# Optimization experiments

Measured on AMD Instinct MI355X. Metric: run time of the kernel, lower is better.

## Reference

```python
import jax, jax.numpy as jnp
import numpy as np

N_MEMORY = 16
FEA_DIM = 512


def setup_inputs() -> dict:
    key = jax.random.key(0)
    ks = jax.random.split(key, 8)
    b, L, d, n = 4, 4096, FEA_DIM, N_MEMORY
    scale = 1.0 / np.sqrt(d)  # ~ torch Linear default init scale
    return {
        "query": jax.random.normal(ks[0], (b, L, d), dtype=jnp.float32),
        "W1": jax.random.uniform(ks[1], (n, d, d), jnp.float32, -scale, scale),
        "b1": jax.random.uniform(ks[2], (n, d), jnp.float32, -scale, scale),
        "W2": jax.random.uniform(ks[3], (n, d, d), jnp.float32, -scale, scale),
        "b2": jax.random.uniform(ks[4], (n, d), jnp.float32, -scale, scale),
        "Wg": jax.random.uniform(ks[5], (n, d), jnp.float32, -scale, scale),
        "bg": jax.random.uniform(ks[6], (n,), jnp.float32, -scale, scale),
        "topk": 8,
    }


def reference(query, W1, b1, W2, b2, Wg, bg, topk):
    # query: [b, L, d]; stacked per-memory-slot params: W1/W2 [n, d, d], Wg [n, d]
    n = W1.shape[0]
    # per-slot LeakyReLU negative slopes: 0.01 + 0.2/n * l
    slopes = (0.01 + 0.2 / n * jnp.arange(n, dtype=query.dtype))[:, None, None, None]
    # memory_function: Linear -> LeakyReLU(slope_l) -> Linear -> Tanh, all slots at once
    h = jnp.einsum('bld,ndh->nblh', query, W1) + b1[:, None, None, :]   # [n,b,L,d]
    h = jnp.where(h >= 0, h, h * slopes)
    x = jnp.tanh(jnp.einsum('nblh,nhd->nbld', h, W2) + b2[:, None, None, :])  # [n,b,L,d]
    # gate: Linear(d,1) -> softmax over L -> topk over L -> gather -> weighted sum
    logits = jnp.einsum('nbld,nd->nbl', x, Wg) + bg[:, None, None]      # [n,b,L]
    w = jax.nn.softmax(logits, axis=-1)
    top_w, top_idx = jax.lax.top_k(w, topk)                             # [n,b,k]
    items = jnp.take_along_axis(x, top_idx[..., None], axis=2)          # [n,b,k,d]
    combined = jnp.einsum('nbkd,nbk->nbd', items, top_w)                # [n,b,d]
    m_item = jnp.transpose(combined, (1, 0, 2))                         # [b,n,d]
    # F.normalize(dim=-1), eps=1e-12
    norm = jnp.maximum(jnp.linalg.norm(m_item, axis=-1, keepdims=True), 1e-12)
    return m_item / norm
```

## Files before the change

kernel.cpp:

```cpp
#include <hip/hip_runtime.h>
#include <hip/hip_bf16.h>
#include <cstdint>
#include <cstddef>

#define NMEM 16
#define DDIM 512
#define BATCH 4
#define LSEQ 4096
#define ROWS 16384
#define NCAND 32
#define KTOP 8
#define QPAD 20

typedef __attribute__((ext_vector_type(4))) float f32x4;
typedef __attribute__((ext_vector_type(16))) float f32x16;
typedef __attribute__((ext_vector_type(8))) int int8v;

__device__ inline void gld16(const void* gptr, void* lptr) {
    __builtin_amdgcn_global_load_lds(
        (const __attribute__((address_space(1))) unsigned int*)gptr,
        (__attribute__((address_space(3))) unsigned int*)lptr,
        16, 0, 0);
}

__device__ inline float fast_tanh(float x) {
    float t = __builtin_amdgcn_fmed3f(x, -3.f, 3.f);
    float t2 = t * t;
    return t * (27.f + t2) * __builtin_amdgcn_rcpf(27.f + 9.f * t2);
}

__device__ inline int8v ldg_frag(const unsigned char* p) {
    int4 x = *(const int4*)p;
    int4 y = *(const int4*)(p + 16);
    int8v v;
    v[0] = x.x; v[1] = x.y; v[2] = x.z; v[3] = x.w;
    v[4] = y.x; v[5] = y.y; v[6] = y.z; v[7] = y.w;
    return v;
}

__device__ inline int8v load_frag_half(const unsigned char* Ts, int row, int kh) {
    int key = (row >> 1) & 3;
    const int4* p0 = (const int4*)(Ts + row * 64 + ((((kh << 1) | 0) ^ key) << 4));
    const int4* p1 = (const int4*)(Ts + row * 64 + ((((kh << 1) | 1) ^ key) << 4));
    int4 x = *p0, y = *p1;
    int8v v;
    v[0] = x.x; v[1] = x.y; v[2] = x.z; v[3] = x.w;
    v[4] = y.x; v[5] = y.y; v[6] = y.z; v[7] = y.w;
    return v;
}

__device__ inline void stage_half(const unsigned char* Wbase, unsigned char* dst,
                                  int tid) {
    #pragma unroll
    for (int i = 0; i < 2; ++i) {
        int c = i * 256 + tid;
        int row = c >> 2, s = c & 3;
        gld16(Wbase + (size_t)row * DDIM + ((s ^ ((row >> 1) & 3)) << 4),
              dst + c * 16);
    }
}

__global__ __launch_bounds__(256)
void prep_kernel(const float* __restrict__ query,
                 const float* __restrict__ W1, const float* __restrict__ W2,
                 unsigned char* __restrict__ Q8,
                 unsigned char* __restrict__ W1T8, unsigned char* __restrict__ W2T8) {
    int blk = blockIdx.x, t = threadIdx.x;
    if (blk < 2048) {
        size_t base = ((size_t)blk * 256 + t) * 16;
        const float4* in = (const float4*)(query + base);
        int4 o; int* op = (int*)&o;
        #pragma unroll
        for (int q = 0; q < 4; ++q) {
            float4 v = in[q];
            int lo = __builtin_amdgcn_cvt_pk_fp8_f32(v.x, v.y, 0, false);
            op[q] = __builtin_amdgcn_cvt_pk_fp8_f32(v.z, v.w, lo, true);
        }
        *(int4*)(Q8 + base) = o;
    } else {
        __shared__ float tile[64][69];
        int bid = blk - 2048;
        const float* Win = W1; unsigned char* Wout = W1T8;
        if (bid >= 1024) { bid -= 1024; Win = W2; Wout = W2T8; }
        int n = bid >> 6, t64 = bid & 63;
        int dt = (t64 >> 3) << 6, jt = (t64 & 7) << 6;
        const float* inN = Win + (size_t)n * DDIM * DDIM;
        unsigned char* outN = Wout + (size_t)n * DDIM * DDIM;
        int rr = t >> 4, cc = (t & 15) * 4;
        #pragma unroll
        for (int pass = 0; pass < 4; ++pass) {
            int row = rr + pass * 16;
            float4 v = *(const float4*)(inN + (size_t)(dt + row) * DDIM + jt + cc);
            tile[row][cc] = v.x; tile[row][cc + 1] = v.y;
            tile[row][cc + 2] = v.z; tile[row][cc + 3] = v.w;
        }
        __syncthreads();
        #pragma unroll
        for (int pass = 0; pass < 4; ++pass) {
            int jl = rr + pass * 16;
            float f0 = tile[cc][jl], f1 = tile[cc + 1][jl];
            float f2 = tile[cc + 2][jl], f3 = tile[cc + 3][jl];
            int lo = __builtin_amdgcn_cvt_pk_fp8_f32(f0, f1, 0, false);
            int dw = __builtin_amdgcn_cvt_pk_fp8_f32(f2, f3, lo, true);
            *(int*)(outN + (size_t)(jt + jl) * DDIM + dt + cc) = dw;
        }
    }
}

__global__ __launch_bounds__(256, 3)
void fused_mlp_kernel(const unsigned char* __restrict__ Q8,
                      const unsigned char* __restrict__ W1T8,
                      const unsigned char* __restrict__ W2T8,
                      const float* __restrict__ b1, const float* __restrict__ b2,
                      const float* __restrict__ Wg,
                      float* __restrict__ logits)
{
    __shared__ unsigned char hbuf[64 * 512];
    __shared__ unsigned char Bs[2][8192];
    __shared__ float lsum[2][64];
    const int id = blockIdx.x;
    const int n = id & 15;
    const int m0 = (id >> 4) * 64;
    const int tid = threadIdx.x, lane = tid & 63;
    const int w = tid >> 6;
    const int rh = w >> 1, ch = w & 1;
    const int l31 = lane & 31, kh = lane >> 5;
    const unsigned char* W1n = W1T8 + (size_t)n * DDIM * DDIM;
    const unsigned char* W2n = W2T8 + (size_t)n * DDIM * DDIM;
    const float slope = 0.01f + 0.0125f * n;
    const unsigned char* Aq0 = Q8 + (size_t)(m0 + rh * 32 + l31) * DDIM + kh * 32;

    int8v avq[8];
    #pragma unroll
    for (int qa = 0; qa < 8; ++qa)
        avq[qa] = ldg_frag(Aq0 + qa * 64);
    stage_half(W1n, Bs[0], tid);
    __syncthreads();

    #pragma unroll 1
    for (int n0 = 0; n0 < 4; ++n0) {
        f32x16 acc[2] = {};
        #pragma unroll
        for (int p8 = 0; p8 < 8; ++p8) {
            const int P = n0 * 8 + p8, Pn = P + 1;
            const unsigned char* nsrc = (Pn < 32)
                ? W1n + (size_t)((Pn >> 3) * 128) * DDIM + (Pn & 7) * 64
                : W2n;
            stage_half(nsrc, Bs[Pn & 1], tid);
            const unsigned char* Ts = Bs[P & 1];
            int8v wfr0 = load_frag_half(Ts, ch * 64 + l31, kh);
            int8v wfr1 = load_frag_half(Ts, ch * 64 + 32 + l31, kh);
            acc[0] = __builtin_amdgcn_mfma_scale_f32_32x32x64_f8f6f4(
                wfr0, avq[p8], acc[0], 0, 0, 0, 0x7F7F7F7F, 0, 0x7F7F7F7F);
            acc[1] = __builtin_amdgcn_mfma_scale_f32_32x32x64_f8f6f4(
                wfr1, avq[p8], acc[1], 0, 0, 0, 0x7F7F7F7F, 0, 0x7F7F7F7F);
            __syncthreads();
        }
        #pragma unroll
        for (int fc = 0; fc < 2; ++fc) {
            int r = rh * 32 + l31;
            #pragma unroll
            for (int q = 0; q < 4; ++q) {
                int jb = n0 * 128 + ch * 64 + fc * 32 + 8 * q + 4 * kh;
                float4 bias = *(const float4*)(b1 + n * DDIM + jb);
                float v0 = acc[fc][4 * q + 0] + bias.x;
                float v1 = acc[fc][4 * q + 1] + bias.y;
                float v2 = acc[fc][4 * q + 2] + bias.z;
                float v3 = acc[fc][4 * q + 3] + bias.w;
                v0 = v0 >= 0.f ? v0 : v0 * slope;
                v1 = v1 >= 0.f ? v1 : v1 * slope;
                v2 = v2 >= 0.f ? v2 : v2 * slope;
                v3 = v3 >= 0.f ? v3 : v3 * slope;
                int lo = __builtin_amdgcn_cvt_pk_fp8_f32(v0, v1, 0, false);
                int dw = __builtin_amdgcn_cvt_pk_fp8_f32(v2, v3, lo, true);
                *(int*)(hbuf + r * 512 + ((((jb >> 4) ^ (r & 7)) << 4) | (jb & 15))) = dw;
            }
        }
    }

    __syncthreads();

    float rowacc[16] = {};
    #pragma unroll 1
    for (int n0 = 0; n0 < 4; ++n0) {
        f32x16 acc[2] = {};
        #pragma unroll 1
        for (int p8 = 0; p8 < 8; ++p8) {
            const int P = 32 + n0 * 8 + p8, Pn = P + 1;
            if (Pn < 64)
                stage_half(W2n + (size_t)(((Pn - 32) >> 3) * 128) * DDIM
                               + ((Pn - 32) & 7) * 64,
                           Bs[Pn & 1], tid);
            int hrow = rh * 32 + l31, hq = hrow & 7;
            int C0 = p8 * 4 + 2 * kh;
            int8v hv;
            {
                const int4* p0 = (const int4*)(hbuf + hrow * 512 + ((C0 ^ hq) << 4));
                const int4* p1 = (const int4*)(hbuf + hrow * 512 + (((C0 + 1) ^ hq) << 4));
                int4 x = *p0, y = *p1;
                hv[0] = x.x; hv[1] = x.y; hv[2] = x.z; hv[3] = x.w;
                hv[4] = y.x; hv[5] = y.y; hv[6] = y.z; hv[7] = y.w;
            }
            const unsigned char* Ts = Bs[P & 1];
            int8v wfr0 = load_frag_half(Ts, ch * 64 + l31, kh);
            int8v wfr1 = load_frag_half(Ts, ch * 64 + 32 + l31, kh);
            acc[0] = __builtin_amdgcn_mfma_scale_f32_32x32x64_f8f6f4(
                hv, wfr0, acc[0], 0, 0, 0, 0x7F7F7F7F, 0, 0x7F7F7F7F);
            acc[1] = __builtin_amdgcn_mfma_scale_f32_32x32x64_f8f6f4(
                hv, wfr1, acc[1], 0, 0, 0, 0x7F7F7F7F, 0, 0x7F7F7F7F);
            __syncthreads();
        }
        #pragma unroll
        for (int fc = 0; fc < 2; ++fc) {
            int j = n0 * 128 + ch * 64 + fc * 32 + l31;
            float bias = b2[n * DDIM + j];
            float wgv = Wg[n * DDIM + j];
            #pragma unroll
            for (int reg = 0; reg < 16; ++reg)
                rowacc[reg] = fmaf(fast_tanh(acc[fc][reg] + bias), wgv, rowacc[reg]);
        }
    }
    #pragma unroll
    for (int sh = 1; sh < 32; sh <<= 1)
        #pragma unroll
        for (int reg = 0; reg < 16; ++reg)
            rowacc[reg] += __shfl_xor(rowacc[reg], sh);
    if (l31 == 0) {
        #pragma unroll
        for (int reg = 0; reg < 16; ++reg)
            lsum[ch][rh * 32 + (reg & 3) + 8 * (reg >> 2) + 4 * kh] = rowacc[reg];
    }
    __syncthreads();
    if (tid < 64)
        logits[(size_t)n * ROWS + m0 + tid] = lsum[0][tid] + lsum[1][tid];
}

__global__ __launch_bounds__(256)
void topcand_kernel(const float* __restrict__ logits, int* __restrict__ cand,
                    float* __restrict__ ex_logit) {
    __shared__ float lv[LSEQ];
    __shared__ float cv[128];
    __shared__ int   ci[128];
    int p = blockIdx.x, n = p >> 2, b = p & 3;
    int t = threadIdx.x, lane = t & 63, w = t >> 6;
    const float* L = logits + (size_t)n * ROWS + (size_t)b * LSEQ;
    for (int i = t; i < LSEQ; i += 256) lv[i] = L[i];
    __syncthreads();
    float mv[16];
    int base = w * 1024;
    #pragma unroll
    for (int j = 0; j < 16; ++j) mv[j] = lv[base + j * 64 + lane];
    for (int rd = 0; rd < 32; ++rd) {
        float best = mv[0]; int bj = 0;
        #pragma unroll
        for (int j = 1; j < 16; ++j)
            if (mv[j] > best) { best = mv[j]; bj = j; }
        int bidx = base + bj * 64 + lane;
        float rv = best; int ridx = bidx;
        #pragma unroll
        for (int s = 1; s < 64; s <<= 1) {
            float ov = __shfl_xor(rv, s); int oi = __shfl_xor(ridx, s);
            if (ov > rv || (ov == rv && oi < ridx)) { rv = ov; ridx = oi; }
        }
        if (lane == 0) { cv[w * 32 + rd] = rv; ci[w * 32 + rd] = ridx; }
        if (ridx == bidx) mv[bj] = -1e30f;
    }
    __syncthreads();
    if (w == 0) {
        float v2[2]; int i2[2];
        #pragma unroll
        for (int k = 0; k < 2; ++k) { v2[k] = cv[k * 64 + lane]; i2[k] = ci[k * 64 + lane]; }
        for (int rd = 0; rd < 32; ++rd) {
            float best = v2[0]; int bi = i2[0]; int bk = 0;
            if (v2[1] > best || (v2[1] == best && i2[1] < bi)) { best = v2[1]; bi = i2[1]; bk = 1; }
            float rv = best; int ridx = bi;
            #pragma unroll
            for (int s = 1; s < 64; s <<= 1) {
                float ov = __shfl_xor(rv, s); int oi = __shfl_xor(ridx, s);
                if (ov > rv || (ov == rv && oi < ridx)) { rv = ov; ridx = oi; }
            }
            if (lane == 0) cand[p * NCAND + rd] = ridx;
            if (ridx == bi) v2[bk] = -1e30f;
        }
    } else if (w == 1) {
        if (lane < NCAND) ex_logit[p * NCAND + lane] = 0.f;
    }
}

__global__ __launch_bounds__(256)
void exact_h_kernel(const float* __restrict__ query,
                    const float* __restrict__ W1, const float* __restrict__ b1,
                    const int* __restrict__ cand, float* __restrict__ ex_h) {
    __shared__ float qs[DDIM][QPAD];
    __shared__ float hpart[4][16][64];
    int blk = blockIdx.x;
    int p = blk >> 4, r4 = blk & 15;
    int ct = r4 >> 3, jc = r4 & 7;
    int n = p >> 2, b = p & 3;
    int t = threadIdx.x, jj = t & 63, dg = t >> 6;
    int j = jc * 64 + jj;
    for (int c = 0; c < 16; ++c) {
        int li = cand[p * NCAND + ct * 16 + c];
        const float* qr = query + ((size_t)b * LSEQ + li) * DDIM;
        for (int d = t; d < DDIM; d += 256) qs[d][c] = qr[d];
    }
    __syncthreads();
    const float* W1n = W1 + (size_t)n * DDIM * DDIM;
    float acc[16] = {};
    for (int d = dg * 128; d < dg * 128 + 128; ++d) {
        float wvv = W1n[(size_t)d * DDIM + j];
        const float4* qv = (const float4*)&qs[d][0];
        #pragma unroll
        for (int c4 = 0; c4 < 4; ++c4) {
            float4 q4 = qv[c4];
            acc[c4 * 4 + 0] = fmaf(q4.x, wvv, acc[c4 * 4 + 0]);
            acc[c4 * 4 + 1] = fmaf(q4.y, wvv, acc[c4 * 4 + 1]);
            acc[c4 * 4 + 2] = fmaf(q4.z, wvv, acc[c4 * 4 + 2]);
            acc[c4 * 4 + 3] = fmaf(q4.w, wvv, acc[c4 * 4 + 3]);
        }
    }
    #pragma unroll
    for (int c = 0; c < 16; ++c) hpart[dg][c][jj] = acc[c];
    __syncthreads();
    const float slope = 0.01f + 0.0125f * n;
    float bias = b1[n * DDIM + j];
    for (int cc = dg; cc < 16; cc += 4) {
        float h = hpart[0][cc][jj] + hpart[1][cc][jj] + hpart[2][cc][jj]
                + hpart[3][cc][jj] + bias;
        h = h >= 0.f ? h : h * slope;
        ex_h[((size_t)p * NCAND + ct * 16 + cc) * DDIM + j] = h;
    }
}

__global__ __launch_bounds__(256)
void exact_x_kernel(const float* __restrict__ ex_h,
                    const float* __restrict__ W2, const float* __restrict__ b2,
                    const float* __restrict__ Wg,
                    float* __restrict__ ex_x, float* __restrict__ ex_logit) {
    __shared__ float hs[DDIM][QPAD];
    __shared__ float xpart[4][16][64];
    int blk = blockIdx.x;
    int p = blk >> 4, r4 = blk & 15;
    int ct = r4 >> 3, jc = r4 & 7;
    int n = p >> 2;
    int t = threadIdx.x, jj = t & 63, dg = t >> 6;
    int j = jc * 64 + jj;
    for (int c = 0; c < 16; ++c) {
        const float* hr = ex_h + ((size_t)p * NCAND + ct * 16 + c) * DDIM;
        for (int d = t; d < DDIM; d += 256) hs[d][c] = hr[d];
    }
    __syncthreads();
    const float* W2n = W2 + (size_t)n * DDIM * DDIM;
    float acc[16] = {};
    for (int d = dg * 128; d < dg * 128 + 128; ++d) {
        float wvv = W2n[(size_t)d * DDIM + j];
        const float4* hv = (const float4*)&hs[d][0];
        #pragma unroll
        for (int c4 = 0; c4 < 4; ++c4) {
            float4 h4 = hv[c4];
            acc[c4 * 4 + 0] = fmaf(h4.x, wvv, acc[c4 * 4 + 0]);
            acc[c4 * 4 + 1] = fmaf(h4.y, wvv, acc[c4 * 4 + 1]);
            acc[c4 * 4 + 2] = fmaf(h4.z, wvv, acc[c4 * 4 + 2]);
            acc[c4 * 4 + 3] = fmaf(h4.w, wvv, acc[c4 * 4 + 3]);
        }
    }
    #pragma unroll
    for (int c = 0; c < 16; ++c) xpart[dg][c][jj] = acc[c];
    __syncthreads();
    float bias = b2[n * DDIM + j];
    float wg = Wg[n * DDIM + j];
    for (int cc = dg; cc < 16; cc += 4) {
        float a = xpart[0][cc][jj] + xpart[1][cc][jj] + xpart[2][cc][jj]
                + xpart[3][cc][jj] + bias;
        float x = tanhf(a);
        ex_x[((size_t)p * NCAND + ct * 16 + cc) * DDIM + j] = x;
        float lp = x * wg;
        #pragma unroll
        for (int s = 1; s < 64; s <<= 1) lp += __shfl_xor(lp, s);
        if (jj == 0) atomicAdd(&ex_logit[p * NCAND + ct * 16 + cc], lp);
    }
}

__global__ __launch_bounds__(64)
void final_kernel(const float* __restrict__ ex_x, const float* __restrict__ ex_logit,
                  const int* __restrict__ cand, float* __restrict__ out)
{
    __shared__ float w8s[KTOP];
    __shared__ int   s8s[KTOP];
    int p = blockIdx.x, n = p >> 2, b = p & 3;
    int t = threadIdx.x;
    float myv = (t < NCAND) ? ex_logit[p * NCAND + t] : -1e30f;
    int myidx = (t < NCAND) ? cand[p * NCAND + t] : 0x7fffffff;
    float lmax = 0.f;
    for (int k = 0; k < KTOP; ++k) {
        float rv = myv; int ridx = myidx; int rl = t;
        #pragma unroll
        for (int s = 1; s < 64; s <<= 1) {
            float ov = __shfl_xor(rv, s); int oi = __shfl_xor(ridx, s); int ol = __shfl_xor(rl, s);
            if (ov > rv || (ov == rv && oi < ridx)) { rv = ov; ridx = oi; rl = ol; }
        }
        if (k == 0) lmax = rv;
        if (t == 0) { w8s[k] = __expf(rv - lmax); s8s[k] = rl; }
        if (t == rl) myv = -1e30f;
    }
    __syncthreads();
    float cvv[8];
    float sq = 0.f;
    int idx = 0;
    for (int d = t; d < DDIM; d += 64, ++idx) {
        float s = 0.f;
        #pragma unroll
        for (int k = 0; k < KTOP; ++k)
            s = fmaf(w8s[k], ex_x[((size_t)p * NCAND + s8s[k]) * DDIM + d], s);
        cvv[idx] = s;
        sq += s * s;
    }
    #pragma unroll
    for (int s = 1; s < 64; s <<= 1) sq += __shfl_xor(sq, s);
    float norm = fmaxf(sqrtf(sq), 1e-12f);
    idx = 0;
    for (int d = t; d < DDIM; d += 64, ++idx)
        out[((size_t)b * NMEM + n) * DDIM + d] = cvv[idx] / norm;
}

extern "C" void kernel_launch(void* const* d_in, const int* in_sizes, int n_in,
                              void* d_out, int out_size, void* d_ws, size_t ws_size,
                              hipStream_t stream)
{
    const float* query = (const float*)d_in[0];
    const float* W1    = (const float*)d_in[1];
    const float* b1    = (const float*)d_in[2];
    const float* W2    = (const float*)d_in[3];
    const float* b2    = (const float*)d_in[4];
    const float* Wg    = (const float*)d_in[5];

    char* ws = (char*)d_ws;
    const size_t MB = 1024 * 1024;
    unsigned char* Q8   = (unsigned char*)(ws);
    unsigned char* W1T8 = (unsigned char*)(ws + 8 * MB);
    unsigned char* W2T8 = (unsigned char*)(ws + 12 * MB);
    float* logits   = (float*)(ws + 16 * MB);
    int*   cand     = (int*)  (ws + 17 * MB);
    float* ex_logit = (float*)(ws + 17 * MB + 16384);
    float* ex_h     = (float*)(ws + 20 * MB);
    float* ex_x     = (float*)(ws + 28 * MB);

    prep_kernel<<<4096, 256, 0, stream>>>(query, W1, W2, Q8, W1T8, W2T8);
    fused_mlp_kernel<<<4096, 256, 0, stream>>>(Q8, W1T8, W2T8, b1, b2, Wg, logits);
    topcand_kernel<<<64, 256, 0, stream>>>(logits, cand, ex_logit);
    exact_h_kernel<<<1024, 256, 0, stream>>>(query, W1, b1, cand, ex_h);
    exact_x_kernel<<<1024, 256, 0, stream>>>(ex_h, W2, b2, Wg, ex_x, ex_logit);
    final_kernel<<<64, 64, 0, stream>>>(ex_x, ex_logit, cand, (float*)d_out);
}
```

Baseline: 460.6 us.

## Halve fused MLP row tile to 32 rows with four column-split waves

Each fused_mlp block now handles 32 query rows instead of 64, so the grid doubles to 8192 blocks. Each of the four waves computes one 32-wide column slice with a single MFMA per step, and the four partial logit sums are reduced through shared memory. The smaller hbuf and accumulator footprint is meant to raise occupancy (launch bounds go from 3 to 4). The cost is that every W1/W2 weight tile staged into LDS is now reused across half as many rows, which doubles weight traffic and the barrier count per output row.

After: 572.5 us. 1.24x slower.

```diff
diff --git a/kernel.cpp b/kernel.cpp
--- a/kernel.cpp
+++ b/kernel.cpp
@@ -107,7 +107,7 @@
     }
 }
 
-__global__ __launch_bounds__(256, 3)
+__global__ __launch_bounds__(256, 4)
 void fused_mlp_kernel(const unsigned char* __restrict__ Q8,
                       const unsigned char* __restrict__ W1T8,
                       const unsigned char* __restrict__ W2T8,
@@ -115,20 +115,19 @@
                       const float* __restrict__ Wg,
                       float* __restrict__ logits)
 {
-    __shared__ unsigned char hbuf[64 * 512];
+    __shared__ unsigned char hbuf[32 * 512];
     __shared__ unsigned char Bs[2][8192];
-    __shared__ float lsum[2][64];
+    __shared__ float lsum[4][32];
     const int id = blockIdx.x;
     const int n = id & 15;
-    const int m0 = (id >> 4) * 64;
+    const int m0 = (id >> 4) * 32;
     const int tid = threadIdx.x, lane = tid & 63;
     const int w = tid >> 6;
-    const int rh = w >> 1, ch = w & 1;
     const int l31 = lane & 31, kh = lane >> 5;
     const unsigned char* W1n = W1T8 + (size_t)n * DDIM * DDIM;
     const unsigned char* W2n = W2T8 + (size_t)n * DDIM * DDIM;
     const float slope = 0.01f + 0.0125f * n;
-    const unsigned char* Aq0 = Q8 + (size_t)(m0 + rh * 32 + l31) * DDIM + kh * 32;
+    const unsigned char* Aq0 = Q8 + (size_t)(m0 + l31) * DDIM + kh * 32;
 
     int8v avq[8];
     #pragma unroll
@@ -139,7 +138,7 @@
 
     #pragma unroll 1
     for (int n0 = 0; n0 < 4; ++n0) {
-        f32x16 acc[2] = {};
+        f32x16 acc = {};
         #pragma unroll
         for (int p8 = 0; p8 < 8; ++p8) {
             const int P = n0 * 8 + p8, Pn = P + 1;
@@ -148,25 +147,21 @@
                 : W2n;
             stage_half(nsrc, Bs[Pn & 1], tid);
             const unsigned char* Ts = Bs[P & 1];
-            int8v wfr0 = load_frag_half(Ts, ch * 64 + l31, kh);
-            int8v wfr1 = load_frag_half(Ts, ch * 64 + 32 + l31, kh);
-            acc[0] = __builtin_amdgcn_mfma_scale_f32_32x32x64_f8f6f4(
-                wfr0, avq[p8], acc[0], 0, 0, 0, 0x7F7F7F7F, 0, 0x7F7F7F7F);
-            acc[1] = __builtin_amdgcn_mfma_scale_f32_32x32x64_f8f6f4(
-                wfr1, avq[p8], acc[1], 0, 0, 0, 0x7F7F7F7F, 0, 0x7F7F7F7F);
+            int8v wfr = load_frag_half(Ts, w * 32 + l31, kh);
+            acc = __builtin_amdgcn_mfma_scale_f32_32x32x64_f8f6f4(
+                wfr, avq[p8], acc, 0, 0, 0, 0x7F7F7F7F, 0, 0x7F7F7F7F);
             __syncthreads();
         }
-        #pragma unroll
-        for (int fc = 0; fc < 2; ++fc) {
-            int r = rh * 32 + l31;
+        {
+            int r = l31;
             #pragma unroll
             for (int q = 0; q < 4; ++q) {
-                int jb = n0 * 128 + ch * 64 + fc * 32 + 8 * q + 4 * kh;
+                int jb = n0 * 128 + w * 32 + 8 * q + 4 * kh;
                 float4 bias = *(const float4*)(b1 + n * DDIM + jb);
-                float v0 = acc[fc][4 * q + 0] + bias.x;
-                float v1 = acc[fc][4 * q + 1] + bias.y;
-                float v2 = acc[fc][4 * q + 2] + bias.z;
-                float v3 = acc[fc][4 * q + 3] + bias.w;
+                float v0 = acc[4 * q + 0] + bias.x;
+                float v1 = acc[4 * q + 1] + bias.y;
+                float v2 = acc[4 * q + 2] + bias.z;
+                float v3 = acc[4 * q + 3] + bias.w;
                 v0 = v0 >= 0.f ? v0 : v0 * slope;
                 v1 = v1 >= 0.f ? v1 : v1 * slope;
                 v2 = v2 >= 0.f ? v2 : v2 * slope;
@@ -183,7 +178,7 @@
     float rowacc[16] = {};
     #pragma unroll 1
     for (int n0 = 0; n0 < 4; ++n0) {
-        f32x16 acc[2] = {};
+        f32x16 acc = {};
         #pragma unroll 1
         for (int p8 = 0; p8 < 8; ++p8) {
             const int P = 32 + n0 * 8 + p8, Pn = P + 1;
@@ -191,7 +186,7 @@
                 stage_half(W2n + (size_t)(((Pn - 32) >> 3) * 128) * DDIM
                                + ((Pn - 32) & 7) * 64,
                            Bs[Pn & 1], tid);
-            int hrow = rh * 32 + l31, hq = hrow & 7;
+            int hrow = l31, hq = hrow & 7;
             int C0 = p8 * 4 + 2 * kh;
             int8v hv;
             {
@@ -202,22 +197,18 @@
                 hv[4] = y.x; hv[5] = y.y; hv[6] = y.z; hv[7] = y.w;
             }
             const unsigned char* Ts = Bs[P & 1];
-            int8v wfr0 = load_frag_half(Ts, ch * 64 + l31, kh);
-            int8v wfr1 = load_frag_half(Ts, ch * 64 + 32 + l31, kh);
-            acc[0] = __builtin_amdgcn_mfma_scale_f32_32x32x64_f8f6f4(
-                hv, wfr0, acc[0], 0, 0, 0, 0x7F7F7F7F, 0, 0x7F7F7F7F);
-            acc[1] = __builtin_amdgcn_mfma_scale_f32_32x32x64_f8f6f4(
-                hv, wfr1, acc[1], 0, 0, 0, 0x7F7F7F7F, 0, 0x7F7F7F7F);
+            int8v wfr = load_frag_half(Ts, w * 32 + l31, kh);
+            acc = __builtin_amdgcn_mfma_scale_f32_32x32x64_f8f6f4(
+                hv, wfr, acc, 0, 0, 0, 0x7F7F7F7F, 0, 0x7F7F7F7F);
             __syncthreads();
         }
-        #pragma unroll
-        for (int fc = 0; fc < 2; ++fc) {
-            int j = n0 * 128 + ch * 64 + fc * 32 + l31;
+        {
+            int j = n0 * 128 + w * 32 + l31;
             float bias = b2[n * DDIM + j];
             float wgv = Wg[n * DDIM + j];
             #pragma unroll
             for (int reg = 0; reg < 16; ++reg)
-                rowacc[reg] = fmaf(fast_tanh(acc[fc][reg] + bias), wgv, rowacc[reg]);
+                rowacc[reg] = fmaf(fast_tanh(acc[reg] + bias), wgv, rowacc[reg]);
         }
     }
     #pragma unroll
@@ -228,11 +219,12 @@
     if (l31 == 0) {
         #pragma unroll
         for (int reg = 0; reg < 16; ++reg)
-            lsum[ch][rh * 32 + (reg & 3) + 8 * (reg >> 2) + 4 * kh] = rowacc[reg];
-    }
-    __syncthreads();
-    if (tid < 64)
-        logits[(size_t)n * ROWS + m0 + tid] = lsum[0][tid] + lsum[1][tid];
+            lsum[w][(reg & 3) + 8 * (reg >> 2) + 4 * kh] = rowacc[reg];
+    }
+    __syncthreads();
+    if (tid < 32)
+        logits[(size_t)n * ROWS + m0 + tid] =
+            lsum[0][tid] + lsum[1][tid] + lsum[2][tid] + lsum[3][tid];
 }
 
 __global__ __launch_bounds__(256)
@@ -446,7 +438,7 @@
     float* ex_x     = (float*)(ws + 28 * MB);
 
     prep_kernel<<<4096, 256, 0, stream>>>(query, W1, W2, Q8, W1T8, W2T8);
-    fused_mlp_kernel<<<4096, 256, 0, stream>>>(Q8, W1T8, W2T8, b1, b2, Wg, logits);
+    fused_mlp_kernel<<<8192, 256, 0, stream>>>(Q8, W1T8, W2T8, b1, b2, Wg, logits);
     topcand_kernel<<<64, 256, 0, stream>>>(logits, cand, ex_logit);
     exact_h_kernel<<<1024, 256, 0, stream>>>(query, W1, b1, cand, ex_h);
     exact_x_kernel<<<1024, 256, 0, stream>>>(ex_h, W2, b2, Wg, ex_x, ex_logit);
```
